# Kernel optimization log

Measured on AMD Instinct MI355X. Metric: run time of the kernel, lower is better.

## Reference

```python
import jax, jax.numpy as jnp
import numpy as np

N_CLASSES = 19


def setup_inputs() -> dict:
    key = jax.random.key(0)
    k1, k2 = jax.random.split(key)
    embedding = jax.random.normal(k1, (4, 32, 128, 128), dtype=jnp.float32)
    label = jax.random.randint(k2, (4, 512, 512), 0, N_CLASSES, dtype=jnp.int64)
    return {"embedding": embedding, "label": label}


def _discriminative_loss(embedding, label, n_classes=N_CLASSES):
    N, H, W = label.shape
    C = embedding.shape[1]
    # bilinear upsample embedding to label resolution (F.upsample mode='bilinear')
    emb = jax.image.resize(embedding, (N, C, H, W), method="bilinear")
    HW = H * W
    emb = emb.reshape(N, C, HW).transpose(0, 2, 1)          # (N, HW, C)
    lab = label.reshape(N, HW)                               # (N, HW)

    onehot = jax.nn.one_hot(lab, n_classes, dtype=emb.dtype)  # (N, HW, K)
    count = onehot.sum(1)                                    # (N, K)
    mask = (count > 0).astype(emb.dtype)                     # (N, K)

    # per-class embedding sum and (biased, /(count+1)) mean
    cls_sum = jnp.einsum("npc,npk->nkc", emb, onehot)       # (N, K, C)
    cls_mean = cls_sum / (count[:, :, None] + 1.0)           # (N, K, C)

    # intra-class: per-pixel squared distance to own-class mean, mean over C
    mean_pp = jnp.take_along_axis(cls_mean, lab[:, :, None], axis=1)  # (N, HW, C)
    d2 = jnp.mean((emb - mean_pp) ** 2, axis=-1)             # (N, HW)
    intra_per_cls = jnp.einsum("np,npk->nk", d2, onehot) / (count + 1.0)  # (N, K)
    n_fg = mask[:, 1:].sum(1)                                # (N,)
    l2_intra = (intra_per_cls[:, 1:] * mask[:, 1:]).sum(1) / n_fg  # (N,)

    # inter-class: pairwise mean squared distance between class means
    diff = cls_mean[:, :, None, :] - cls_mean[:, None, :, :]  # (N, K, K, C)
    inter = jnp.mean(diff ** 2, axis=-1)                     # (N, K, K)
    inter = inter * mask[:, None, :] * mask[:, :, None]
    l2_inter = inter[:, 1:, 1:].reshape(N, -1).sum(1) / (n_fg * n_fg)  # (N,)

    return l2_intra - l2_inter


def reference(embedding, label):
    return _discriminative_loss(embedding, label)
```

## Files before the change

### kernel.cpp

```cpp
#include <hip/hip_runtime.h>

#define NIMG 4
#define NCLS 19
#define CCH  32
#define LH   128
#define LW   128
#define HH   512
#define WW   512
#define HWQ  (LH*LW)
#define HWP  (HH*WW)

#define TR 8
#define TC 16
#define NTILE 128
#define TCELLS 128
#define HALO_R 36
#define HALO_C 68
#define QROWS 128

#define L_ET  0
#define L_A   4224
#define L_RED 6656
#define LDS_FLOATS 9088

__device__ __forceinline__ void taps(int v, int lim, int& i0, int& i1, float& f) {
    int r = v & 3;
    int b = (v >> 2) + ((r < 2) ? -1 : 0);
    f = 0.125f + 0.25f * (float)((r + 2) & 3);
    i0 = b < 0 ? 0 : b;
    i1 = (b + 1 > lim) ? lim : (b + 1);
}

__global__ __launch_bounds__(256) void k_main(const float* __restrict__ E,
        const int* __restrict__ lab, float* __restrict__ P_sum,
        float* __restrict__ P_cnt, float* __restrict__ P_S2) {
    __shared__ float lds[LDS_FLOATS];
    const int n = blockIdx.y;
    const int tid = threadIdx.x;

    if (blockIdx.x < NTILE) {
        const int tile = blockIdx.x;
        const int ty = tile >> 3, tx = tile & 7;
        const int Y0 = ty * TR, X0 = tx * TC;

        for (int i = tid; i < TCELLS * NCLS; i += 256) lds[L_A + i] = 0.f;
#pragma unroll
        for (int it = 0; it < 16; it++) {
            int idx = it * 256 + tid;
            int c = idx >> 7, cell = idx & 127;
            int cy = cell >> 4, cx = cell & 15;
            float e = E[((size_t)n * CCH + c) * HWQ + (Y0 + cy) * LW + (X0 + cx)];
            lds[L_ET + cell * 33 + c] = e;
        }
        __syncthreads();

        const int* ln = lab + (size_t)n * HWP;
        int h_lo = Y0 * 4 - 2, w_lo = X0 * 4 - 2;
        for (int i = tid; i < HALO_R * HALO_C; i += 256) {
            int hr = i / HALO_C, wc = i - hr * HALO_C;
            int h = h_lo + hr, w = w_lo + wc;
            if (h < 0 || h >= HH || w < 0 || w >= WW) continue;
            int L = ln[h * WW + w];
            int y0, y1, x0, x1; float fy, fx;
            taps(h, LH - 1, y0, y1, fy);
            taps(w, LW - 1, x0, x1, fx);
            int yy[2] = {y0, y1}; float wy[2] = {1.f - fy, fy};
            int xx[2] = {x0, x1}; float wx[2] = {1.f - fx, fx};
#pragma unroll
            for (int a = 0; a < 2; a++) {
#pragma unroll
                for (int b = 0; b < 2; b++) {
                    int ry = yy[a] - Y0, rx = xx[b] - X0;
                    if (ry >= 0 && ry < TR && rx >= 0 && rx < TC)
                        atomicAdd(&lds[L_A + (ry * TC + rx) * NCLS + L], wy[a] * wx[b]);
                }
            }
        }
        __syncthreads();

        const int g = tid >> 5, c = tid & 31;
        float acc[NCLS];
#pragma unroll
        for (int k = 0; k < NCLS; k++) acc[k] = 0.f;
#pragma unroll
        for (int j = 0; j < 16; j++) {
            int cell = g * 16 + j;
            float e = lds[L_ET + cell * 33 + c];
            const float* Ar = &lds[L_A + cell * NCLS];
#pragma unroll
            for (int k = 0; k < NCLS; k++) acc[k] = fmaf(Ar[k], e, acc[k]);
        }
#pragma unroll
        for (int k = 0; k < NCLS; k++) acc[k] += __shfl_xor(acc[k], 32);
        const int wave = tid >> 6;
        if ((tid & 63) < 32) {
#pragma unroll
            for (int k = 0; k < NCLS; k++)
                lds[L_RED + wave * 608 + k * 32 + c] = acc[k];
        }
        __syncthreads();

        float* Ps = P_sum + (size_t)(n * NTILE + tile) * (NCLS * CCH);
        for (int i = tid; i < NCLS * CCH; i += 256) {
            float s = lds[L_RED + i] + lds[L_RED + 608 + i]
                    + lds[L_RED + 1216 + i] + lds[L_RED + 1824 + i];
            Ps[i] = s;
        }
        if (tid < NCLS) {
            float s = 0.f;
            for (int cell = 0; cell < TCELLS; cell++) s += lds[L_A + cell * NCLS + tid];
            P_cnt[((size_t)n * NCLS + tid) * NTILE + tile] = s;
        }
    } else {
        const int by = blockIdx.x - NTILE;
        const int half = tid >> 7, bx = tid & 127;
        if (tid < NCLS) lds[tid] = 0.f;
        __syncthreads();

        const float* En = E + ((size_t)n * CCH + half * 16) * HWQ;
        int r0 = (by == 0) ? 0 : by - 1;
        int r2 = (by == LH - 1) ? LH - 1 : by + 1;
        int c0 = (bx == 0) ? 0 : bx - 1;
        int c2 = (bx == LW - 1) ? LW - 1 : bx + 1;
        int o0 = r0 * LW, o1 = by * LW, o2 = r2 * LW;

        float d2[16];
#pragma unroll
        for (int i = 0; i < 16; i++) d2[i] = 0.f;

#pragma unroll
        for (int c = 0; c < 16; c++) {
            const float* Ep = En + (size_t)c * HWQ;
            float e00 = Ep[o0 + c0], e01 = Ep[o0 + bx], e02 = Ep[o0 + c2];
            float e10 = Ep[o1 + c0], e11 = Ep[o1 + bx], e12 = Ep[o1 + c2];
            float e20 = Ep[o2 + c0], e21 = Ep[o2 + bx], e22 = Ep[o2 + c2];
            float dy0 = e10 - e00, dy1 = e11 - e01, dy2 = e12 - e02;
            float dz0 = e20 - e10, dz1 = e21 - e11, dz2 = e22 - e12;
            float ry[4][3];
            ry[0][0] = fmaf(0.625f, dy0, e00); ry[0][1] = fmaf(0.625f, dy1, e01); ry[0][2] = fmaf(0.625f, dy2, e02);
            ry[1][0] = fmaf(0.875f, dy0, e00); ry[1][1] = fmaf(0.875f, dy1, e01); ry[1][2] = fmaf(0.875f, dy2, e02);
            ry[2][0] = fmaf(0.125f, dz0, e10); ry[2][1] = fmaf(0.125f, dz1, e11); ry[2][2] = fmaf(0.125f, dz2, e12);
            ry[3][0] = fmaf(0.375f, dz0, e10); ry[3][1] = fmaf(0.375f, dz1, e11); ry[3][2] = fmaf(0.375f, dz2, e12);
#pragma unroll
            for (int r = 0; r < 4; r++) {
                float da = ry[r][1] - ry[r][0], db = ry[r][2] - ry[r][1];
                float v0 = fmaf(0.625f, da, ry[r][0]);
                float v1 = fmaf(0.875f, da, ry[r][0]);
                float v2 = fmaf(0.125f, db, ry[r][1]);
                float v3 = fmaf(0.375f, db, ry[r][1]);
                d2[r * 4 + 0] = fmaf(v0, v0, d2[r * 4 + 0]);
                d2[r * 4 + 1] = fmaf(v1, v1, d2[r * 4 + 1]);
                d2[r * 4 + 2] = fmaf(v2, v2, d2[r * 4 + 2]);
                d2[r * 4 + 3] = fmaf(v3, v3, d2[r * 4 + 3]);
            }
        }
        const int* lp = lab + (size_t)n * HWP + (by * 4) * WW + bx * 4;
#pragma unroll
        for (int r = 0; r < 4; r++) {
            int4 l4 = *(const int4*)(lp + r * WW);
            atomicAdd(&lds[l4.x], d2[r * 4 + 0]);
            atomicAdd(&lds[l4.y], d2[r * 4 + 1]);
            atomicAdd(&lds[l4.z], d2[r * 4 + 2]);
            atomicAdd(&lds[l4.w], d2[r * 4 + 3]);
        }
        __syncthreads();
        if (tid < NCLS)
            P_S2[((size_t)n * NCLS + tid) * QROWS + by] = lds[tid];
    }
}

__global__ __launch_bounds__(640) void k_final(const float* __restrict__ P_sum,
        const float* __restrict__ P_cnt, const float* __restrict__ P_S2,
        float* __restrict__ out) {
    const int n = blockIdx.x, t = threadIdx.x;
    __shared__ float csum[NCLS * 33];
    __shared__ float m[NCLS * 33];
    __shared__ float cnt[NCLS];
    __shared__ float S2[NCLS];
    __shared__ float sIntra, sNfg, sInter;
    if (t == 0) sInter = 0.f;

    if (t < NCLS * CCH) {
        const int k = t >> 5, c = t & 31;
        const float* p = P_sum + (size_t)n * NTILE * (NCLS * CCH) + t;
        float s = 0.f;
        for (int b = 0; b < NTILE; b++) s += p[b * (NCLS * CCH)];
        csum[k * 33 + c] = s;
        const float* pc = P_cnt + ((size_t)n * NCLS + k) * NTILE;
        float sc = pc[c] + pc[c + 32] + pc[c + 64] + pc[c + 96];
        const float* ps = P_S2 + ((size_t)n * NCLS + k) * QROWS;
        float s2 = ps[c] + ps[c + 32] + ps[c + 64] + ps[c + 96];
#pragma unroll
        for (int mk = 16; mk >= 1; mk >>= 1) {
            sc += __shfl_xor(sc, mk);
            s2 += __shfl_xor(s2, mk);
        }
        if (c == 0) { cnt[k] = sc; S2[k] = s2; }
    }
    __syncthreads();
    if (t < NCLS * CCH) {
        const int k = t >> 5, c = t & 31;
        m[k * 33 + c] = csum[k * 33 + c] / (cnt[k] + 1.f);
    }
    __syncthreads();

    float vi = 0.f, fg = 0.f;
    if (t >= 1 && t < NCLS && cnt[t] > 0.f) {
        fg = 1.f;
        float dot = 0.f, mm = 0.f;
#pragma unroll
        for (int c = 0; c < CCH; c++) {
            float mv = m[t * 33 + c];
            dot = fmaf(mv, csum[t * 33 + c], dot);
            mm = fmaf(mv, mv, mm);
        }
        vi = (S2[t] - 2.f * dot + cnt[t] * mm) * (1.f / 32.f) / (cnt[t] + 1.f);
    }
#pragma unroll
    for (int s_ = 32; s_ >= 1; s_ >>= 1) { vi += __shfl_xor(vi, s_); fg += __shfl_xor(fg, s_); }
    if (t == 0) { sIntra = vi; sNfg = fg; }

    float ve = 0.f;
    if (t < 324) {
        int j = 1 + t / 18, k = 1 + t % 18;
        if (cnt[j] > 0.f && cnt[k] > 0.f) {
            float s = 0.f;
#pragma unroll
            for (int c = 0; c < CCH; c++) {
                float d = m[j * 33 + c] - m[k * 33 + c];
                s = fmaf(d, d, s);
            }
            ve = s * (1.f / 32.f);
        }
    }
#pragma unroll
    for (int s_ = 32; s_ >= 1; s_ >>= 1) ve += __shfl_xor(ve, s_);
    if ((t & 63) == 0) atomicAdd(&sInter, ve);
    __syncthreads();
    if (t == 0) out[n] = sIntra / sNfg - sInter / (sNfg * sNfg);
}

extern "C" void kernel_launch(void* const* d_in, const int* in_sizes, int n_in,
                              void* d_out, int out_size, void* d_ws, size_t ws_size,
                              hipStream_t stream) {
    const float* E = (const float*)d_in[0];
    const int* lab = (const int*)d_in[1];
    float* out = (float*)d_out;

    float* ws = (float*)d_ws;
    float* P_sum = ws;
    float* P_cnt = P_sum + (size_t)NIMG * NTILE * NCLS * CCH;
    float* P_S2  = P_cnt + (size_t)NIMG * NCLS * NTILE;

    k_main <<<dim3(NTILE + QROWS, NIMG), dim3(256), 0, stream>>>(E, lab, P_sum, P_cnt, P_S2);
    k_final<<<dim3(NIMG), dim3(640), 0, stream>>>(P_sum, P_cnt, P_S2, out);
}
```

Before: 120.1 us.

## Fuse final reduction into main kernel via last-block counter, vectorize loads and LDS layout

Merges the separate finalize kernel into the main kernel: the last block per image, found with an atomic done counter, performs the reduction, and a memset resets the counter each launch. The class-weight matrix in LDS is transposed to a class-major layout with padded stride so the accumulation loop can read float4 values. Embedding tiles are loaded with float4 vector loads. The intra-distance blocks now stage rows in LDS instead of issuing nine scattered global loads per channel. Label loads are hoisted into registers, and per-wave LDS accumulators reduce atomic contention. This removes a kernel launch and memory traffic, at the cost of a memset, a serialized tail block and higher LDS use.

```diff
diff --git a/kernel.cpp b/kernel.cpp
--- a/kernel.cpp
+++ b/kernel.cpp
@@ -13,15 +13,24 @@
 #define TR 8
 #define TC 16
 #define NTILE 128
-#define TCELLS 128
 #define HALO_R 36
 #define HALO_C 68
+#define NHALO (HALO_R*HALO_C)
 #define QROWS 128
+#define NBLK (NTILE+QROWS)
+#define ASTR 132
 
 #define L_ET  0
 #define L_A   4224
-#define L_RED 6656
-#define LDS_FLOATS 9088
+#define L_RED 6732
+#define LDS_FLOATS 9164
+#define L_QS   0
+#define L_QACC 6336
+#define F_CSUM 0
+#define F_M    640
+#define F_CNT  1280
+#define F_S2   1312
+#define F_SC   1344
 
 __device__ __forceinline__ void taps(int v, int lim, int& i0, int& i1, float& f) {
     int r = v & 3;
@@ -31,213 +40,262 @@
     i1 = (b + 1 > lim) ? lim : (b + 1);
 }
 
-__global__ __launch_bounds__(256) void k_main(const float* __restrict__ E,
+__global__ __launch_bounds__(256, 4) void k_main(const float* __restrict__ E,
         const int* __restrict__ lab, float* __restrict__ P_sum,
-        float* __restrict__ P_cnt, float* __restrict__ P_S2) {
+        float* __restrict__ P_cnt, float* __restrict__ P_S2,
+        int* __restrict__ done, float* __restrict__ out) {
     __shared__ float lds[LDS_FLOATS];
+    __shared__ int sLast;
     const int n = blockIdx.y;
     const int tid = threadIdx.x;
-
-    if (blockIdx.x < NTILE) {
-        const int tile = blockIdx.x;
-        const int ty = tile >> 3, tx = tile & 7;
+    const int bid = blockIdx.x;
+
+    if (bid < NTILE) {
+        const int ty = bid >> 3, tx = bid & 7;
         const int Y0 = ty * TR, X0 = tx * TC;
-
-        for (int i = tid; i < TCELLS * NCLS; i += 256) lds[L_A + i] = 0.f;
-#pragma unroll
-        for (int it = 0; it < 16; it++) {
-            int idx = it * 256 + tid;
-            int c = idx >> 7, cell = idx & 127;
-            int cy = cell >> 4, cx = cell & 15;
-            float e = E[((size_t)n * CCH + c) * HWQ + (Y0 + cy) * LW + (X0 + cx)];
-            lds[L_ET + cell * 33 + c] = e;
-        }
-        __syncthreads();
-
+        for (int i = tid; i < NCLS * ASTR; i += 256) lds[L_A + i] = 0.f;
+#pragma unroll
+        for (int it = 0; it < 4; it++) {
+            int seg = it * 256 + tid;
+            int c = seg >> 5, q = seg & 31;
+            int cy = q >> 2, cx = (q & 3) * 4;
+            const float4 ev = *(const float4*)(E + ((size_t)n * CCH + c) * HWQ
+                                               + (Y0 + cy) * LW + X0 + cx);
+            int cell = cy * TC + cx;
+            lds[L_ET + (cell + 0) * 33 + c] = ev.x;
+            lds[L_ET + (cell + 1) * 33 + c] = ev.y;
+            lds[L_ET + (cell + 2) * 33 + c] = ev.z;
+            lds[L_ET + (cell + 3) * 33 + c] = ev.w;
+        }
         const int* ln = lab + (size_t)n * HWP;
-        int h_lo = Y0 * 4 - 2, w_lo = X0 * 4 - 2;
-        for (int i = tid; i < HALO_R * HALO_C; i += 256) {
+        const int h_lo = Y0 * 4 - 2, w_lo = X0 * 4 - 2;
+        int Lv[10];
+#pragma unroll
+        for (int it = 0; it < 10; it++) {
+            int i = it * 256 + tid;
             int hr = i / HALO_C, wc = i - hr * HALO_C;
             int h = h_lo + hr, w = w_lo + wc;
-            if (h < 0 || h >= HH || w < 0 || w >= WW) continue;
-            int L = ln[h * WW + w];
+            bool ok = (i < NHALO) & (h >= 0) & (h < HH) & (w >= 0) & (w < WW);
+            int hc = h < 0 ? 0 : (h > HH - 1 ? HH - 1 : h);
+            int wl = w < 0 ? 0 : (w > WW - 1 ? WW - 1 : w);
+            int lv = ln[hc * WW + wl];
+            Lv[it] = ok ? lv : -1;
+        }
+        __syncthreads();
+#pragma unroll
+        for (int it = 0; it < 10; it++) {
+            if (Lv[it] < 0) continue;
+            int i = it * 256 + tid;
+            int hr = i / HALO_C, wc = i - hr * HALO_C;
+            int h = h_lo + hr, w = w_lo + wc;
             int y0, y1, x0, x1; float fy, fx;
             taps(h, LH - 1, y0, y1, fy);
             taps(w, LW - 1, x0, x1, fx);
             int yy[2] = {y0, y1}; float wy[2] = {1.f - fy, fy};
             int xx[2] = {x0, x1}; float wx[2] = {1.f - fx, fx};
+            float* Ar = &lds[L_A + Lv[it] * ASTR];
 #pragma unroll
             for (int a = 0; a < 2; a++) {
 #pragma unroll
                 for (int b = 0; b < 2; b++) {
                     int ry = yy[a] - Y0, rx = xx[b] - X0;
                     if (ry >= 0 && ry < TR && rx >= 0 && rx < TC)
-                        atomicAdd(&lds[L_A + (ry * TC + rx) * NCLS + L], wy[a] * wx[b]);
+                        atomicAdd(&Ar[ry * TC + rx], wy[a] * wx[b]);
                 }
             }
         }
         __syncthreads();
-
         const int g = tid >> 5, c = tid & 31;
         float acc[NCLS];
 #pragma unroll
         for (int k = 0; k < NCLS; k++) acc[k] = 0.f;
 #pragma unroll
-        for (int j = 0; j < 16; j++) {
-            int cell = g * 16 + j;
-            float e = lds[L_ET + cell * 33 + c];
-            const float* Ar = &lds[L_A + cell * NCLS];
-#pragma unroll
-            for (int k = 0; k < NCLS; k++) acc[k] = fmaf(Ar[k], e, acc[k]);
+        for (int j4 = 0; j4 < 4; j4++) {
+            int cell0 = g * 16 + j4 * 4;
+            float e0 = lds[L_ET + (cell0 + 0) * 33 + c];
+            float e1 = lds[L_ET + (cell0 + 1) * 33 + c];
+            float e2 = lds[L_ET + (cell0 + 2) * 33 + c];
+            float e3 = lds[L_ET + (cell0 + 3) * 33 + c];
+#pragma unroll
+            for (int k = 0; k < NCLS; k++) {
+                const float4 a = *(const float4*)&lds[L_A + k * ASTR + cell0];
+                acc[k] = fmaf(a.x, e0, fmaf(a.y, e1, fmaf(a.z, e2, fmaf(a.w, e3, acc[k]))));
+            }
         }
 #pragma unroll
         for (int k = 0; k < NCLS; k++) acc[k] += __shfl_xor(acc[k], 32);
-        const int wave = tid >> 6;
+        const int wv = tid >> 6;
         if ((tid & 63) < 32) {
 #pragma unroll
-            for (int k = 0; k < NCLS; k++)
-                lds[L_RED + wave * 608 + k * 32 + c] = acc[k];
+            for (int k = 0; k < NCLS; k++) lds[L_RED + wv * 608 + k * 32 + c] = acc[k];
         }
         __syncthreads();
-
-        float* Ps = P_sum + (size_t)(n * NTILE + tile) * (NCLS * CCH);
-        for (int i = tid; i < NCLS * CCH; i += 256) {
-            float s = lds[L_RED + i] + lds[L_RED + 608 + i]
-                    + lds[L_RED + 1216 + i] + lds[L_RED + 1824 + i];
-            Ps[i] = s;
-        }
+        float* Ps = P_sum + (size_t)(n * NTILE + bid) * 608;
+        for (int i = tid; i < 608; i += 256)
+            Ps[i] = lds[L_RED + i] + lds[L_RED + 608 + i]
+                  + lds[L_RED + 1216 + i] + lds[L_RED + 1824 + i];
         if (tid < NCLS) {
             float s = 0.f;
-            for (int cell = 0; cell < TCELLS; cell++) s += lds[L_A + cell * NCLS + tid];
-            P_cnt[((size_t)n * NCLS + tid) * NTILE + tile] = s;
+#pragma unroll
+            for (int q = 0; q < 32; q++) {
+                const float4 a = *(const float4*)&lds[L_A + tid * ASTR + q * 4];
+                s += a.x + a.y + a.z + a.w;
+            }
+            P_cnt[((size_t)n * NCLS + tid) * NTILE + bid] = s;
         }
     } else {
-        const int by = blockIdx.x - NTILE;
-        const int half = tid >> 7, bx = tid & 127;
-        if (tid < NCLS) lds[tid] = 0.f;
+        const int by = bid - NTILE;
+        const int grp = tid >> 7, bx = tid & 127;
+        if ((tid & 63) < 20) lds[L_QACC + (tid >> 6) * 20 + (tid & 63)] = 0.f;
+        const int r0 = (by == 0) ? 0 : by - 1;
+        const int r2 = (by == LH - 1) ? LH - 1 : by + 1;
+        const int xm = (bx == 0) ? 0 : bx - 1;
+        const int xp = (bx == LW - 1) ? LW - 1 : bx + 1;
+        float d2[16];
+#pragma unroll
+        for (int i = 0; i < 16; i++) d2[i] = 0.f;
+        const float* En = E + (size_t)n * CCH * HWQ;
+
+#pragma unroll
+        for (int half = 0; half < 2; half++) {
+            __syncthreads();
+#pragma unroll
+            for (int it = 0; it < 6; it++) {
+                int seg = it * 256 + tid;
+                int rowid = seg >> 5, x4 = (seg & 31) * 4;
+                int c = rowid / 3, r = rowid - c * 3;
+                int row = (r == 0) ? r0 : ((r == 1) ? by : r2);
+                const float4 ev = *(const float4*)(En + (size_t)(half * 16 + c) * HWQ
+                                                   + row * LW + x4);
+                *(float4*)&lds[L_QS + rowid * ASTR + x4] = ev;
+            }
+            __syncthreads();
+#pragma unroll
+            for (int j = 0; j < 8; j++) {
+                const float* R0 = &lds[L_QS + ((grp * 8 + j) * 3) * ASTR];
+                const float* R1 = R0 + ASTR;
+                const float* R2 = R1 + ASTR;
+                float e00 = R0[xm], e01 = R0[bx], e02 = R0[xp];
+                float e10 = R1[xm], e11 = R1[bx], e12 = R1[xp];
+                float e20 = R2[xm], e21 = R2[bx], e22 = R2[xp];
+                float dy0 = e10 - e00, dy1 = e11 - e01, dy2 = e12 - e02;
+                float dz0 = e20 - e10, dz1 = e21 - e11, dz2 = e22 - e12;
+                float ry[4][3];
+                ry[0][0] = fmaf(0.625f, dy0, e00); ry[0][1] = fmaf(0.625f, dy1, e01); ry[0][2] = fmaf(0.625f, dy2, e02);
+                ry[1][0] = fmaf(0.875f, dy0, e00); ry[1][1] = fmaf(0.875f, dy1, e01); ry[1][2] = fmaf(0.875f, dy2, e02);
+                ry[2][0] = fmaf(0.125f, dz0, e10); ry[2][1] = fmaf(0.125f, dz1, e11); ry[2][2] = fmaf(0.125f, dz2, e12);
+                ry[3][0] = fmaf(0.375f, dz0, e10); ry[3][1] = fmaf(0.375f, dz1, e11); ry[3][2] = fmaf(0.375f, dz2, e12);
+#pragma unroll
+                for (int r = 0; r < 4; r++) {
+                    float da = ry[r][1] - ry[r][0], db = ry[r][2] - ry[r][1];
+                    float v0 = fmaf(0.625f, da, ry[r][0]);
+                    float v1 = fmaf(0.875f, da, ry[r][0]);
+                    float v2 = fmaf(0.125f, db, ry[r][1]);
+                    float v3 = fmaf(0.375f, db, ry[r][1]);
+                    d2[r * 4 + 0] = fmaf(v0, v0, d2[r * 4 + 0]);
+                    d2[r * 4 + 1] = fmaf(v1, v1, d2[r * 4 + 1]);
+                    d2[r * 4 + 2] = fmaf(v2, v2, d2[r * 4 + 2]);
+                    d2[r * 4 + 3] = fmaf(v3, v3, d2[r * 4 + 3]);
+                }
+            }
+        }
+        const int* lp = lab + (size_t)n * HWP + (by * 4) * WW + bx * 4;
+        int4 lv[4];
+#pragma unroll
+        for (int r = 0; r < 4; r++) lv[r] = *(const int4*)(lp + r * WW);
+        float* accW = &lds[L_QACC + (tid >> 6) * 20];
+#pragma unroll
+        for (int r = 0; r < 4; r++) {
+            atomicAdd(&accW[lv[r].x], d2[r * 4 + 0]);
+            atomicAdd(&accW[lv[r].y], d2[r * 4 + 1]);
+            atomicAdd(&accW[lv[r].z], d2[r * 4 + 2]);
+            atomicAdd(&accW[lv[r].w], d2[r * 4 + 3]);
+        }
         __syncthreads();
-
-        const float* En = E + ((size_t)n * CCH + half * 16) * HWQ;
-        int r0 = (by == 0) ? 0 : by - 1;
-        int r2 = (by == LH - 1) ? LH - 1 : by + 1;
-        int c0 = (bx == 0) ? 0 : bx - 1;
-        int c2 = (bx == LW - 1) ? LW - 1 : bx + 1;
-        int o0 = r0 * LW, o1 = by * LW, o2 = r2 * LW;
-
-        float d2[16];
-#pragma unroll
-        for (int i = 0; i < 16; i++) d2[i] = 0.f;
-
-#pragma unroll
-        for (int c = 0; c < 16; c++) {
-            const float* Ep = En + (size_t)c * HWQ;
-            float e00 = Ep[o0 + c0], e01 = Ep[o0 + bx], e02 = Ep[o0 + c2];
-            float e10 = Ep[o1 + c0], e11 = Ep[o1 + bx], e12 = Ep[o1 + c2];
-            float e20 = Ep[o2 + c0], e21 = Ep[o2 + bx], e22 = Ep[o2 + c2];
-            float dy0 = e10 - e00, dy1 = e11 - e01, dy2 = e12 - e02;
-            float dz0 = e20 - e10, dz1 = e21 - e11, dz2 = e22 - e12;
-            float ry[4][3];
-            ry[0][0] = fmaf(0.625f, dy0, e00); ry[0][1] = fmaf(0.625f, dy1, e01); ry[0][2] = fmaf(0.625f, dy2, e02);
-            ry[1][0] = fmaf(0.875f, dy0, e00); ry[1][1] = fmaf(0.875f, dy1, e01); ry[1][2] = fmaf(0.875f, dy2, e02);
-            ry[2][0] = fmaf(0.125f, dz0, e10); ry[2][1] = fmaf(0.125f, dz1, e11); ry[2][2] = fmaf(0.125f, dz2, e12);
-            ry[3][0] = fmaf(0.375f, dz0, e10); ry[3][1] = fmaf(0.375f, dz1, e11); ry[3][2] = fmaf(0.375f, dz2, e12);
-#pragma unroll
-            for (int r = 0; r < 4; r++) {
-                float da = ry[r][1] - ry[r][0], db = ry[r][2] - ry[r][1];
-                float v0 = fmaf(0.625f, da, ry[r][0]);
-                float v1 = fmaf(0.875f, da, ry[r][0]);
-                float v2 = fmaf(0.125f, db, ry[r][1]);
-                float v3 = fmaf(0.375f, db, ry[r][1]);
-                d2[r * 4 + 0] = fmaf(v0, v0, d2[r * 4 + 0]);
-                d2[r * 4 + 1] = fmaf(v1, v1, d2[r * 4 + 1]);
-                d2[r * 4 + 2] = fmaf(v2, v2, d2[r * 4 + 2]);
-                d2[r * 4 + 3] = fmaf(v3, v3, d2[r * 4 + 3]);
-            }
-        }
-        const int* lp = lab + (size_t)n * HWP + (by * 4) * WW + bx * 4;
-#pragma unroll
-        for (int r = 0; r < 4; r++) {
-            int4 l4 = *(const int4*)(lp + r * WW);
-            atomicAdd(&lds[l4.x], d2[r * 4 + 0]);
-            atomicAdd(&lds[l4.y], d2[r * 4 + 1]);
-            atomicAdd(&lds[l4.z], d2[r * 4 + 2]);
-            atomicAdd(&lds[l4.w], d2[r * 4 + 3]);
-        }
-        __syncthreads();
-        if (tid < NCLS)
-            P_S2[((size_t)n * NCLS + tid) * QROWS + by] = lds[tid];
-    }
-}
-
-__global__ __launch_bounds__(640) void k_final(const float* __restrict__ P_sum,
-        const float* __restrict__ P_cnt, const float* __restrict__ P_S2,
-        float* __restrict__ out) {
-    const int n = blockIdx.x, t = threadIdx.x;
-    __shared__ float csum[NCLS * 33];
-    __shared__ float m[NCLS * 33];
-    __shared__ float cnt[NCLS];
-    __shared__ float S2[NCLS];
-    __shared__ float sIntra, sNfg, sInter;
-    if (t == 0) sInter = 0.f;
-
-    if (t < NCLS * CCH) {
-        const int k = t >> 5, c = t & 31;
-        const float* p = P_sum + (size_t)n * NTILE * (NCLS * CCH) + t;
-        float s = 0.f;
-        for (int b = 0; b < NTILE; b++) s += p[b * (NCLS * CCH)];
-        csum[k * 33 + c] = s;
+        if (tid < NCLS) {
+            float s = lds[L_QACC + tid] + lds[L_QACC + 20 + tid]
+                    + lds[L_QACC + 40 + tid] + lds[L_QACC + 60 + tid];
+            P_S2[((size_t)n * NCLS + tid) * QROWS + by] = s;
+        }
+    }
+
+    __threadfence();
+    __syncthreads();
+    if (tid == 0) {
+        int old = atomicAdd(&done[n], 1);
+        sLast = (old == NBLK - 1) ? 1 : 0;
+        if (sLast) __threadfence();
+    }
+    __syncthreads();
+    if (!sLast) return;
+
+    const float* Ps = P_sum + (size_t)n * NTILE * 608;
+    for (int base = 0; base < 608; base += 256) {
+        int idx = base + tid;
+        if (idx < 608) {
+            float s = 0.f;
+#pragma unroll 4
+            for (int b = 0; b < NTILE; b++) s += Ps[(size_t)b * 608 + idx];
+            lds[F_CSUM + (idx >> 5) * 33 + (idx & 31)] = s;
+        }
+    }
+    if (tid < 152) {
+        int k = tid >> 3, j = tid & 7;
         const float* pc = P_cnt + ((size_t)n * NCLS + k) * NTILE;
-        float sc = pc[c] + pc[c + 32] + pc[c + 64] + pc[c + 96];
         const float* ps = P_S2 + ((size_t)n * NCLS + k) * QROWS;
-        float s2 = ps[c] + ps[c + 32] + ps[c + 64] + ps[c + 96];
-#pragma unroll
-        for (int mk = 16; mk >= 1; mk >>= 1) {
-            sc += __shfl_xor(sc, mk);
-            s2 += __shfl_xor(s2, mk);
-        }
-        if (c == 0) { cnt[k] = sc; S2[k] = s2; }
-    }
-    __syncthreads();
-    if (t < NCLS * CCH) {
-        const int k = t >> 5, c = t & 31;
-        m[k * 33 + c] = csum[k * 33 + c] / (cnt[k] + 1.f);
-    }
-    __syncthreads();
-
+        float sc = 0.f, s2 = 0.f;
+        for (int i = j; i < NTILE; i += 8) { sc += pc[i]; s2 += ps[i]; }
+        sc += __shfl_xor(sc, 4); sc += __shfl_xor(sc, 2); sc += __shfl_xor(sc, 1);
+        s2 += __shfl_xor(s2, 4); s2 += __shfl_xor(s2, 2); s2 += __shfl_xor(s2, 1);
+        if (j == 0) { lds[F_CNT + k] = sc; lds[F_S2 + k] = s2; }
+    }
+    if (tid == 0) lds[F_SC + 2] = 0.f;
+    __syncthreads();
+    for (int base = 0; base < 608; base += 256) {
+        int idx = base + tid;
+        if (idx < 608) {
+            int k = idx >> 5, c = idx & 31;
+            lds[F_M + k * 33 + c] = lds[F_CSUM + k * 33 + c] / (lds[F_CNT + k] + 1.f);
+        }
+    }
+    __syncthreads();
     float vi = 0.f, fg = 0.f;
-    if (t >= 1 && t < NCLS && cnt[t] > 0.f) {
+    if (tid >= 1 && tid < NCLS && lds[F_CNT + tid] > 0.f) {
         fg = 1.f;
+        float ct = lds[F_CNT + tid];
         float dot = 0.f, mm = 0.f;
 #pragma unroll
         for (int c = 0; c < CCH; c++) {
-            float mv = m[t * 33 + c];
-            dot = fmaf(mv, csum[t * 33 + c], dot);
+            float mv = lds[F_M + tid * 33 + c];
+            dot = fmaf(mv, lds[F_CSUM + tid * 33 + c], dot);
             mm = fmaf(mv, mv, mm);
         }
-        vi = (S2[t] - 2.f * dot + cnt[t] * mm) * (1.f / 32.f) / (cnt[t] + 1.f);
+        vi = (lds[F_S2 + tid] - 2.f * dot + ct * mm) * (1.f / 32.f) / (ct + 1.f);
     }
 #pragma unroll
     for (int s_ = 32; s_ >= 1; s_ >>= 1) { vi += __shfl_xor(vi, s_); fg += __shfl_xor(fg, s_); }
-    if (t == 0) { sIntra = vi; sNfg = fg; }
-
+    if (tid == 0) { lds[F_SC] = vi; lds[F_SC + 1] = fg; }
     float ve = 0.f;
-    if (t < 324) {
-        int j = 1 + t / 18, k = 1 + t % 18;
-        if (cnt[j] > 0.f && cnt[k] > 0.f) {
+    for (int p = tid; p < 324; p += 256) {
+        int j = 1 + p / 18, k = 1 + p % 18;
+        if (lds[F_CNT + j] > 0.f && lds[F_CNT + k] > 0.f) {
             float s = 0.f;
 #pragma unroll
             for (int c = 0; c < CCH; c++) {
-                float d = m[j * 33 + c] - m[k * 33 + c];
+                float d = lds[F_M + j * 33 + c] - lds[F_M + k * 33 + c];
                 s = fmaf(d, d, s);
             }
-            ve = s * (1.f / 32.f);
+            ve += s * (1.f / 32.f);
         }
     }
 #pragma unroll
     for (int s_ = 32; s_ >= 1; s_ >>= 1) ve += __shfl_xor(ve, s_);
-    if ((t & 63) == 0) atomicAdd(&sInter, ve);
-    __syncthreads();
-    if (t == 0) out[n] = sIntra / sNfg - sInter / (sNfg * sNfg);
+    if ((tid & 63) == 0) atomicAdd(&lds[F_SC + 2], ve);
+    __syncthreads();
+    if (tid == 0) {
+        float nfg = lds[F_SC + 1];
+        out[n] = lds[F_SC] / nfg - lds[F_SC + 2] / (nfg * nfg);
+    }
 }
 
 extern "C" void kernel_launch(void* const* d_in, const int* in_sizes, int n_in,
@@ -247,11 +305,11 @@
     const int* lab = (const int*)d_in[1];
     float* out = (float*)d_out;
 
-    float* ws = (float*)d_ws;
-    float* P_sum = ws;
+    int* done = (int*)d_ws;
+    float* P_sum = (float*)d_ws + 16;
     float* P_cnt = P_sum + (size_t)NIMG * NTILE * NCLS * CCH;
     float* P_S2  = P_cnt + (size_t)NIMG * NCLS * NTILE;
 
-    k_main <<<dim3(NTILE + QROWS, NIMG), dim3(256), 0, stream>>>(E, lab, P_sum, P_cnt, P_S2);
-    k_final<<<dim3(NIMG), dim3(640), 0, stream>>>(P_sum, P_cnt, P_S2, out);
+    hipMemsetAsync(d_ws, 0, 16, stream);
+    k_main<<<dim3(NBLK, NIMG), dim3(256), 0, stream>>>(E, lab, P_sum, P_cnt, P_S2, done, out);
 }
```

New measurement: 196.2 us. +63.4%, slower.
